# Kernel tuning notes

Hardware: AMD Instinct MI355X
Metric: run time of the kernel (lower is better)

The kernel has to match this reference:

```python
import jax, jax.numpy as jnp
import numpy as np

WH, WW = 7, 7           # window height/width
N = WH * WW             # tokens per window = 49
C = 768                 # num_channels
H = 24                  # num_heads
D = C // H              # head_dim = 32
B = 1024                # total windows (batch * windows-per-image)
NW = 64                 # windows per image (shift_mask leading dim)
EPS = 1e-5


def _relative_position_index():
    # Mirrors the torch buffer construction in __init__.
    coords = np.stack(np.meshgrid(np.arange(WH), np.arange(WW), indexing='ij'))  # [2,WH,WW]
    cf = coords.reshape(2, -1)                          # [2,N]
    rel = cf[:, :, None] - cf[:, None, :]               # [2,N,N]
    rel = rel.transpose(1, 2, 0).copy()                 # [N,N,2]
    rel[:, :, 0] += WH - 1
    rel[:, :, 1] += WW - 1
    rel[:, :, 0] *= 2 * WW - 1
    return jnp.asarray(rel.sum(-1), dtype=jnp.int32)    # [N,N]


def setup_inputs() -> dict:
    key = jax.random.key(0)
    ks = jax.random.split(key, 6)
    x = jax.random.normal(ks[0], (B, N, C), dtype=jnp.float32)
    shift_mask = jax.random.normal(ks[1], (NW, N, N), dtype=jnp.float32)
    w_qkv = jax.random.normal(ks[2], (3 * C, C), dtype=jnp.float32) * 0.02
    b_qkv = jnp.zeros((3 * C,), dtype=jnp.float32)
    w_proj = jax.random.normal(ks[3], (C, C), dtype=jnp.float32) * 0.02
    b_proj = jnp.zeros((C,), dtype=jnp.float32)
    rel_bias_table = jax.random.normal(ks[4], ((2 * WH - 1) * (2 * WW - 1), H), dtype=jnp.float32) * 0.02
    ln_g = jnp.ones((C,), dtype=jnp.float32)
    ln_b = jnp.zeros((C,), dtype=jnp.float32)
    rel_pos_index = _relative_position_index()
    return {
        'x': x, 'shift_mask': shift_mask,
        'w_qkv': w_qkv, 'b_qkv': b_qkv,
        'w_proj': w_proj, 'b_proj': b_proj,
        'rel_bias_table': rel_bias_table,
        'ln_g': ln_g, 'ln_b': ln_b,
        'rel_pos_index': rel_pos_index,
    }


def reference(x, shift_mask, w_qkv, b_qkv, w_proj, b_proj, rel_bias_table, ln_g, ln_b, rel_pos_index):
    B_, N_, C_ = x.shape
    # QKV projection: [B,N,3C] -> [3,B,H,N,D]
    qkv = (x @ w_qkv.T + b_qkv).reshape(B_, N_, 3, H, D).transpose(2, 0, 3, 1, 4)
    q, k, v = qkv[0], qkv[1], qkv[2]
    # Relative position bias gather: [N,N,H] -> [1,H,N,N]
    bias = rel_bias_table[rel_pos_index.reshape(-1)].reshape(N_, N_, H).transpose(2, 0, 1)[None]
    # Shift mask broadcast over batch repeats and heads: [B,1,N,N]
    mask = jnp.tile(shift_mask, (B_ // shift_mask.shape[0], 1, 1))[:, None]
    attn_bias = bias + mask  # [B,H,N,N]
    scale = 1.0 / np.sqrt(D).astype(np.float32)
    scores = jnp.einsum('bhnd,bhmd->bhnm', q, k) * scale + attn_bias
    attn = jax.nn.softmax(scores, axis=-1)
    out = jnp.einsum('bhnm,bhmd->bhnd', attn, v)       # [B,H,N,D]
    out = out.transpose(0, 2, 1, 3).reshape(B_, N_, C_)
    out = out @ w_proj.T + b_proj                      # dropout p=0 -> identity
    y = out + x
    mu = jnp.mean(y, axis=-1, keepdims=True)
    var = jnp.mean(jnp.square(y - mu), axis=-1, keepdims=True)
    return (y - mu) * jax.lax.rsqrt(var + EPS) * ln_g + ln_b
```

## Files before the change

kernel.cpp:

```cpp
#include <hip/hip_runtime.h>
#include <hip/hip_bf16.h>

#define SEQ 49
#define CH 768
#define NH 24
#define HD 32
#define NB 1024
#define NWIN 64
#define MTOT (NB*SEQ)

typedef __hip_bfloat16 bf16;
typedef __attribute__((ext_vector_type(8))) short short8;
typedef __attribute__((ext_vector_type(4))) short short4v;
typedef __attribute__((ext_vector_type(4))) float f32x4;

#define MD  ((size_t)MTOT * HD)
#define NHMD ((size_t)NH * MD)

__device__ __forceinline__ void gload16(const void* g, void* l) {
  __builtin_amdgcn_global_load_lds((__attribute__((address_space(1))) void*)g,
                                   (__attribute__((address_space(3))) void*)l,
                                   16, 0, 0);
}

__device__ __forceinline__ float bf2f(short s) {
  return __uint_as_float(((unsigned int)(unsigned short)s) << 16);
}

__global__ void cvt_bf16(const float* __restrict__ in, bf16* __restrict__ o, int n4) {
  int i = blockIdx.x * blockDim.x + threadIdx.x;
  if (i >= n4) return;
  float4 v = ((const float4*)in)[i];
  union { bf16 b[4]; short4 s; } u;
  u.b[0] = __float2bfloat16(v.x);
  u.b[1] = __float2bfloat16(v.y);
  u.b[2] = __float2bfloat16(v.z);
  u.b[3] = __float2bfloat16(v.w);
  ((short4*)o)[i] = u.s;
}

__global__ void build_comb(const float* __restrict__ table, const int* __restrict__ rpi,
                           const float* __restrict__ smask, bf16* __restrict__ comb) {
  int i = blockIdx.x * blockDim.x + threadIdx.x;
  if (i >= NWIN * NH * 1024) return;
  int idx = i * 4;
  int e0 = idx & 7;
  int l = (idx >> 3) & 63;
  int jj = (idx >> 9) & 7;
  int sh = idx >> 12;
  int h = sh % NH;
  int s = sh / NH;
  union { bf16 b[4]; short4 v; } u;
#pragma unroll
  for (int k = 0; k < 4; k++) {
    int j = jj * 8 + e0 + k;
    int mt = j >> 4, nt = (j >> 2) & 3, r = j & 3;
    int m = 16 * mt + 4 * (l >> 4) + r;
    int n = 16 * nt + (l & 15);
    float v = -1e30f;
    if (m < SEQ && n < SEQ)
      v = (table[rpi[m * SEQ + n] * NH + h] + smask[s * SEQ * SEQ + m * SEQ + n])
          * 1.4426950408889634f;
    u.b[k] = __float2bfloat16(v);
  }
  *(short4*)(comb + idx) = u.v;
}

__global__ __launch_bounds__(512) void qkv_gemm(
    const bf16* __restrict__ A, const bf16* __restrict__ Bw,
    const float* __restrict__ bias, bf16* __restrict__ C)
{
  extern __shared__ __align__(16) bf16 lds[];
  const int tid = threadIdx.x;
  const int w = tid >> 6, l = tid & 63;
  const int lr = l & 15, lg = l >> 4;
  const int wm = w >> 2, wn = w & 3;

  const int flat = blockIdx.x;
  const int xcd = flat & 7, lid = flat >> 3;
  const int wgid = (xcd < 4 ? xcd * 221 : 884 + (xcd - 4) * 220) + lid;
  const int bm = wgid / 9, bn = wgid - 9 * bm;

  const bf16* gA[4];
  const bf16* gB[4];
  int ldst[4];
#pragma unroll
  for (int j = 0; j < 4; j++) {
    int c = j * 512 + tid;
    int row = c >> 3, cpos = c & 7;
    int srcch = cpos ^ (row & 7);
    gA[j] = A + ((size_t)(bm * 256 + row)) * CH + srcch * 8;
    gB[j] = Bw + ((size_t)(bn * 256 + row)) * CH + srcch * 8;
    ldst[j] = c * 8;
  }

  f32x4 acc[8][4];
  f32x4 zero4 = {0.f, 0.f, 0.f, 0.f};
#pragma unroll
  for (int i = 0; i < 8; i++)
#pragma unroll
    for (int j = 0; j < 4; j++) acc[i][j] = zero4;

  int offA[8][2], offB[4][2];
#pragma unroll
  for (int mi = 0; mi < 8; mi++)
#pragma unroll
    for (int ks = 0; ks < 2; ks++) {
      int rowa = wm * 128 + mi * 16 + lr;
      offA[mi][ks] = rowa * 64 + ((lg + 4 * ks) ^ (rowa & 7)) * 8;
    }
#pragma unroll
  for (int nj = 0; nj < 4; nj++)
#pragma unroll
    for (int ks = 0; ks < 2; ks++) {
      int rowb = wn * 64 + nj * 16 + lr;
      offB[nj][ks] = rowb * 64 + ((lg + 4 * ks) ^ (rowb & 7)) * 8;
    }

  gload16(gB[0], lds + 32768 + ldst[0]);
  gload16(gB[1], lds + 32768 + ldst[1]);
  gload16(gB[2], lds + 32768 + ldst[2]);
  gload16(gB[3], lds + 32768 + ldst[3]);
  gload16(gA[0], lds + ldst[0]);
  gload16(gA[2], lds + ldst[2]);
  gload16(gA[1], lds + ldst[1]);
  gload16(gA[3], lds + ldst[3]);

  for (int t = 0; t < 12; ++t) {
    const int cur = t & 1;
    const bf16* cA = lds + cur * 16384;
    const bf16* cB = lds + 32768 + cur * 16384;
    bf16* nA = lds + (cur ^ 1) * 16384;
    bf16* nB = lds + 32768 + (cur ^ 1) * 16384;
    const int kk = (t + 1) * 64;
    const bool pf = (t < 11);
#pragma unroll
    for (int p = 0; p < 4; ++p) {
      const int hp = p >> 1, ks = p & 1;
      if (p == 0) {
        asm volatile("s_waitcnt vmcnt(2)" ::: "memory");
      } else if (p == 2) {
        if (pf) asm volatile("s_waitcnt vmcnt(4)" ::: "memory");
        else    asm volatile("s_waitcnt vmcnt(0)" ::: "memory");
      }
      __builtin_amdgcn_sched_barrier(0);
      __builtin_amdgcn_s_barrier();
      __builtin_amdgcn_sched_barrier(0);
      short8 af[4], bfv[4];
#pragma unroll
      for (int mi = 0; mi < 4; mi++) af[mi] = *(const short8*)(cA + offA[hp * 4 + mi][ks]);
#pragma unroll
      for (int nj = 0; nj < 4; nj++) bfv[nj] = *(const short8*)(cB + offB[nj][ks]);
      if (pf) {
        if (p == 0) { gload16(gB[0] + kk, nB + ldst[0]); gload16(gB[1] + kk, nB + ldst[1]); }
        if (p == 1) { gload16(gB[2] + kk, nB + ldst[2]); gload16(gB[3] + kk, nB + ldst[3]); }
        if (p == 2) { gload16(gA[0] + kk, nA + ldst[0]); gload16(gA[2] + kk, nA + ldst[2]); }
        if (p == 3) { gload16(gA[1] + kk, nA + ldst[1]); gload16(gA[3] + kk, nA + ldst[3]); }
      }
      asm volatile("s_waitcnt lgkmcnt(0)" ::: "memory");
      __builtin_amdgcn_sched_barrier(0);
      __builtin_amdgcn_s_setprio(1);
#pragma unroll
      for (int mi = 0; mi < 4; mi++)
#pragma unroll
        for (int nj = 0; nj < 4; nj++)
          acc[hp * 4 + mi][nj] =
              __builtin_amdgcn_mfma_f32_16x16x32_bf16(af[mi], bfv[nj], acc[hp * 4 + mi][nj], 0, 0, 0);
      __builtin_amdgcn_s_setprio(0);
    }
  }

  const float scale = 0.25503487724583985f;
  const int colbase = bn * 256 + 64 * wn;
  const int rowbase = bm * 256 + 128 * wm;
#pragma unroll
  for (int nj = 0; nj < 4; nj++) {
    const int cb16 = colbase + 16 * nj;
    const int sec = cb16 / 768;
    const int rem = cb16 - sec * 768;
    const int h = rem >> 5;
    const int dbase = rem & 31;
    float bv = bias[cb16 + lr];
    if (sec == 2) {
      const size_t vbase = 2 * NHMD + ((size_t)h * HD + dbase + lr) * MTOT;
#pragma unroll
      for (int mi = 0; mi < 8; mi++) {
        size_t row = rowbase + 16 * mi + 4 * lg;
        union { bf16 b[4]; short4 s; } u;
#pragma unroll
        for (int r = 0; r < 4; r++) u.b[r] = __float2bfloat16(acc[mi][nj][r] + bv);
        *(short4*)(C + vbase + row) = u.s;
      }
    } else {
      const float mul = (sec == 0) ? scale : 1.0f;
      const size_t base = (size_t)sec * NHMD + (size_t)h * MD + dbase + lr;
#pragma unroll
      for (int mi = 0; mi < 8; mi++) {
#pragma unroll
        for (int r = 0; r < 4; r++) {
          size_t row = rowbase + 16 * mi + 4 * lg + r;
          C[base + row * HD] = __float2bfloat16((acc[mi][nj][r] + bv) * mul);
        }
      }
    }
  }
}

__global__ __launch_bounds__(256, 4) void attn_kernel(
    const bf16* __restrict__ qkvT, const bf16* __restrict__ comb,
    bf16* __restrict__ aout)
{
  __shared__ __align__(16) bf16 P[4][64 * 72];
  const int tid = threadIdx.x;
  const int w = tid >> 6, l = tid & 63;
  const int lr = l & 15, lg = l >> 4;
  const int b = blockIdx.x;
  const int h = blockIdx.y * 4 + w;
  const size_t rowb = (size_t)b * SEQ;
  f32x4 zero4 = {0.f, 0.f, 0.f, 0.f};

  const bf16* qb = qkvT + (size_t)h * MD + rowb * HD;
  const bf16* kb = qkvT + NHMD + (size_t)h * MD + rowb * HD;
  const bf16* vT = qkvT + 2 * NHMD + (size_t)h * HD * MTOT;

  short8 kf[4];
#pragma unroll
  for (int nt = 0; nt < 4; nt++)
    kf[nt] = *(const short8*)(kb + (16 * nt + lr) * HD + 8 * lg);

  short8 pb[2][2];
#pragma unroll
  for (int kt = 0; kt < 2; kt++)
#pragma unroll
    for (int dt = 0; dt < 2; dt++)
      pb[kt][dt] = *(const short8*)(vT + ((size_t)(16 * dt + lr)) * MTOT + rowb + 32 * kt + 8 * lg);

  const bf16* cbp = comb + (((size_t)(b & (NWIN - 1)) * NH + h) << 12);
  float inv[4][4];

#pragma unroll
  for (int mt = 0; mt < 4; mt++) {
    short8 qf = *(const short8*)(qb + (16 * mt + lr) * HD + 8 * lg);
    f32x4 s4[4];
#pragma unroll
    for (int nt = 0; nt < 4; nt++)
      s4[nt] = __builtin_amdgcn_mfma_f32_16x16x32_bf16(qf, kf[nt], zero4, 0, 0, 0);
    short8 c0 = *(const short8*)(cbp + ((2 * mt) * 64 + l) * 8);
    short8 c1 = *(const short8*)(cbp + ((2 * mt + 1) * 64 + l) * 8);
#pragma unroll
    for (int e = 0; e < 8; e++) s4[e >> 2][e & 3] += bf2f(c0[e]);
#pragma unroll
    for (int e = 0; e < 8; e++) s4[2 + (e >> 2)][e & 3] += bf2f(c1[e]);
#pragma unroll
    for (int r = 0; r < 4; r++) {
      float t = 0.f;
#pragma unroll
      for (int nt = 0; nt < 4; nt++) {
        float e = exp2f(s4[nt][r]);
        s4[nt][r] = e;
        t += e;
      }
      t += __shfl_xor(t, 1, 64);
      t += __shfl_xor(t, 2, 64);
      t += __shfl_xor(t, 4, 64);
      t += __shfl_xor(t, 8, 64);
      inv[mt][r] = 1.0f / t;
    }
#pragma unroll
    for (int nt = 0; nt < 4; nt++)
#pragma unroll
      for (int r = 0; r < 4; r++)
        P[w][(16 * mt + 4 * lg + r) * 72 + 16 * nt + lr] = __float2bfloat16(s4[nt][r]);
  }

  f32x4 o[4][2];
#pragma unroll
  for (int mt = 0; mt < 4; mt++) { o[mt][0] = zero4; o[mt][1] = zero4; }
#pragma unroll
  for (int kt = 0; kt < 2; kt++) {
    short8 pa[4];
#pragma unroll
    for (int mt = 0; mt < 4; mt++)
      pa[mt] = *(const short8*)(&P[w][(16 * mt + lr) * 72 + 32 * kt + 8 * lg]);
#pragma unroll
    for (int mt = 0; mt < 4; mt++)
#pragma unroll
      for (int dt = 0; dt < 2; dt++)
        o[mt][dt] = __builtin_amdgcn_mfma_f32_16x16x32_bf16(pa[mt], pb[kt][dt], o[mt][dt], 0, 0, 0);
  }

#pragma unroll
  for (int mt = 0; mt < 4; mt++)
#pragma unroll
    for (int dt = 0; dt < 2; dt++)
#pragma unroll
      for (int r = 0; r < 4; r++) {
        int m = 16 * mt + 4 * lg + r;
        if (m < SEQ)
          aout[(rowb + m) * CH + h * HD + 16 * dt + lr] =
              __float2bfloat16(o[mt][dt][r] * inv[mt][r]);
      }
}

__global__ __launch_bounds__(256) void proj_gemm(
    const bf16* __restrict__ A, const bf16* __restrict__ Bw,
    const float* __restrict__ bias, const bf16* __restrict__ xb,
    bf16* __restrict__ Y)
{
  __shared__ __align__(16) bf16 As[2 * 128 * 64];
  __shared__ __align__(16) bf16 Bs[2 * 128 * 64];
  const int tid = threadIdx.x;
  const int w = tid >> 6, l = tid & 63;
  const int lr = l & 15, lg = l >> 4;
  const int wm = w >> 1, wn = w & 1;

  const int flat = blockIdx.x;
  const int wg = (flat & 7) * 294 + (flat >> 3);
  const int bm = wg / 6, bn = wg - 6 * (wg / 6);

  const bf16* gA[4];
  const bf16* gB[4];
  int ldst[4];
#pragma unroll
  for (int j = 0; j < 4; j++) {
    int c = j * 256 + tid;
    int row = c >> 3, cpos = c & 7;
    int srcch = cpos ^ (row & 7);
    gA[j] = A + ((size_t)(bm * 128 + row)) * CH + srcch * 8;
    gB[j] = Bw + ((size_t)(bn * 128 + row)) * CH + srcch * 8;
    ldst[j] = c * 8;
  }

  f32x4 acc[4][4];
  f32x4 zero4 = {0.f, 0.f, 0.f, 0.f};
#pragma unroll
  for (int i = 0; i < 4; i++)
#pragma unroll
    for (int j = 0; j < 4; j++) acc[i][j] = zero4;

  int offA[4][2], offB[4][2];
#pragma unroll
  for (int mi = 0; mi < 4; mi++) {
#pragma unroll
    for (int ks = 0; ks < 2; ks++) {
      int rowa = 64 * wm + 16 * mi + lr;
      offA[mi][ks] = rowa * 64 + ((lg + 4 * ks) ^ (rowa & 7)) * 8;
      int rowb = 64 * wn + 16 * mi + lr;
      offB[mi][ks] = rowb * 64 + ((lg + 4 * ks) ^ (rowb & 7)) * 8;
    }
  }

#pragma unroll
  for (int j = 0; j < 4; j++) gload16(gA[j], As + ldst[j]);
#pragma unroll
  for (int j = 0; j < 4; j++) gload16(gB[j], Bs + ldst[j]);

  for (int t = 0; t < 12; ++t) {
    const int base = (t & 1) * 8192;
    asm volatile("s_waitcnt vmcnt(0)" ::: "memory");
    __builtin_amdgcn_sched_barrier(0);
    __builtin_amdgcn_s_barrier();
    __builtin_amdgcn_sched_barrier(0);
    const bf16* cA = As + base;
    const bf16* cB = Bs + base;
    bf16* nA = As + (base ^ 8192);
    bf16* nB = Bs + (base ^ 8192);
    const int kk = (t + 1) * 64;
    const bool pf = (t < 11);
#pragma unroll
    for (int ks = 0; ks < 2; ks++) {
      short8 af[4], bfv[4];
#pragma unroll
      for (int mi = 0; mi < 4; mi++) {
        af[mi] = *(const short8*)(cA + offA[mi][ks]);
        bfv[mi] = *(const short8*)(cB + offB[mi][ks]);
      }
      if (pf && ks == 0) {
#pragma unroll
        for (int j = 0; j < 4; j++) {
          gload16(gA[j] + kk, nA + ldst[j]);
          gload16(gB[j] + kk, nB + ldst[j]);
        }
      }
      asm volatile("s_waitcnt lgkmcnt(0)" ::: "memory");
      __builtin_amdgcn_sched_barrier(0);
      __builtin_amdgcn_s_setprio(1);
#pragma unroll
      for (int mi = 0; mi < 4; mi++)
#pragma unroll
        for (int nj = 0; nj < 4; nj++)
          acc[mi][nj] = __builtin_amdgcn_mfma_f32_16x16x32_bf16(af[mi], bfv[nj], acc[mi][nj], 0, 0, 0);
      __builtin_amdgcn_s_setprio(0);
    }
  }

  const int colbase = bn * 128 + 64 * wn;
  const int rowbase = bm * 128 + 64 * wm;
#pragma unroll
  for (int nj = 0; nj < 4; nj++) {
    int col = colbase + 16 * nj + lr;
    float bv = bias[col];
#pragma unroll
    for (int mi = 0; mi < 4; mi++) {
#pragma unroll
      for (int r = 0; r < 4; r++) {
        size_t row = rowbase + 16 * mi + 4 * lg + r;
        float v = acc[mi][nj][r] + bv + bf2f(((const short*)xb)[row * CH + col]);
        Y[row * CH + col] = __float2bfloat16(v);
      }
    }
  }
}

__global__ __launch_bounds__(256) void ln_kernel(
    const bf16* __restrict__ Y, const float* __restrict__ g,
    const float* __restrict__ be, float* __restrict__ out)
{
  const int w = threadIdx.x >> 6, l = threadIdx.x & 63;
  const size_t r = (size_t)blockIdx.x * 4 + w;
  const bf16* yr = Y + r * CH;

  short8 a = *(const short8*)(yr + 8 * l);
  short4v b4 = *(const short4v*)(yr + 512 + 4 * l);
  float v[12];
#pragma unroll
  for (int j = 0; j < 8; j++) v[j] = bf2f(a[j]);
#pragma unroll
  for (int j = 0; j < 4; j++) v[8 + j] = bf2f(b4[j]);

  float s1 = 0.f, s2 = 0.f;
#pragma unroll
  for (int j = 0; j < 12; j++) { s1 += v[j]; s2 += v[j] * v[j]; }
#pragma unroll
  for (int m = 1; m <= 32; m <<= 1) {
    s1 += __shfl_xor(s1, m, 64);
    s2 += __shfl_xor(s2, m, 64);
  }
  float mu = s1 * (1.0f / 768.0f);
  float var = s2 * (1.0f / 768.0f) - mu * mu;
  float rs = rsqrtf(var + 1e-5f);

  float4 g0 = *(const float4*)(g + 8 * l);
  float4 g1 = *(const float4*)(g + 8 * l + 4);
  float4 g2 = *(const float4*)(g + 512 + 4 * l);
  float4 b0 = *(const float4*)(be + 8 * l);
  float4 b1 = *(const float4*)(be + 8 * l + 4);
  float4 b2 = *(const float4*)(be + 512 + 4 * l);

  float4 o0, o1, o2;
  o0.x = (v[0] - mu) * rs * g0.x + b0.x;
  o0.y = (v[1] - mu) * rs * g0.y + b0.y;
  o0.z = (v[2] - mu) * rs * g0.z + b0.z;
  o0.w = (v[3] - mu) * rs * g0.w + b0.w;
  o1.x = (v[4] - mu) * rs * g1.x + b1.x;
  o1.y = (v[5] - mu) * rs * g1.y + b1.y;
  o1.z = (v[6] - mu) * rs * g1.z + b1.z;
  o1.w = (v[7] - mu) * rs * g1.w + b1.w;
  o2.x = (v[8] - mu) * rs * g2.x + b2.x;
  o2.y = (v[9] - mu) * rs * g2.y + b2.y;
  o2.z = (v[10] - mu) * rs * g2.z + b2.z;
  o2.w = (v[11] - mu) * rs * g2.w + b2.w;

  float* orow = out + r * CH;
  *(float4*)(orow + 8 * l) = o0;
  *(float4*)(orow + 8 * l + 4) = o1;
  *(float4*)(orow + 512 + 4 * l) = o2;
}

extern "C" void kernel_launch(void* const* d_in, const int* in_sizes, int n_in,
                              void* d_out, int out_size, void* d_ws, size_t ws_size,
                              hipStream_t stream) {
  (void)in_sizes; (void)n_in; (void)out_size; (void)ws_size;
  const float* x     = (const float*)d_in[0];
  const float* smask = (const float*)d_in[1];
  const float* wqkv  = (const float*)d_in[2];
  const float* bqkv  = (const float*)d_in[3];
  const float* wproj = (const float*)d_in[4];
  const float* bproj = (const float*)d_in[5];
  const float* table = (const float*)d_in[6];
  const float* lng   = (const float*)d_in[7];
  const float* lnb   = (const float*)d_in[8];
  const int*   rpi   = (const int*)d_in[9];
  float* out = (float*)d_out;

  char* ws = (char*)d_ws;
  bf16*  xb   = (bf16*)(ws);
  bf16*  wqb  = (bf16*)(ws + 77070336);
  bf16*  wpb  = (bf16*)(ws + 80609280);
  bf16*  comb = (bf16*)(ws + 81788928);
  bf16*  qkvT = (bf16*)(ws + 94371840);
  bf16*  aout = (bf16*)(ws + 325582848);
  bf16*  yb   = (bf16*)(ws + 94371840);

  cvt_bf16<<<37632, 256, 0, stream>>>(x, xb, 9633792);
  cvt_bf16<<<1728, 256, 0, stream>>>(wqkv, wqb, 442368);
  cvt_bf16<<<576, 256, 0, stream>>>(wproj, wpb, 147456);
  build_comb<<<6144, 256, 0, stream>>>(table, rpi, smask, comb);
  qkv_gemm<<<1764, 512, 131072, stream>>>(xb, wqb, bqkv, qkvT);
  attn_kernel<<<dim3(1024, 6), 256, 0, stream>>>(qkvT, comb, aout);
  proj_gemm<<<2352, 256, 0, stream>>>(aout, wpb, bproj, xb, yb);
  ln_kernel<<<12544, 256, 0, stream>>>(yb, lng, lnb, out);
}
```

Measured before the change: 512.7 us.

## Split GEMM k-step into four phases with staggered partial vmcnt waits

The projection GEMM main loop is restructured into four sub-phases per k-tile, each with a barrier. The next tile's global-to-LDS loads are spread across the phases, and the code waits on partial vmcnt counts so MFMA work can begin before the full tile has landed. The attention kernel also hoists all four Q fragment loads ahead of the score loop. The changes trade more barriers and tighter reasoning about load ordering for better overlap of memory and compute, and they risk LDS hazards if the vmcnt counts are wrong.

```diff
diff --git a/kernel.cpp b/kernel.cpp
--- a/kernel.cpp
+++ b/kernel.cpp
@@ -223,7 +223,10 @@
   const bf16* kb = qkvT + NHMD + (size_t)h * MD + rowb * HD;
   const bf16* vT = qkvT + 2 * NHMD + (size_t)h * HD * MTOT;
 
-  short8 kf[4];
+  short8 qf[4], kf[4];
+#pragma unroll
+  for (int mt = 0; mt < 4; mt++)
+    qf[mt] = *(const short8*)(qb + (16 * mt + lr) * HD + 8 * lg);
 #pragma unroll
   for (int nt = 0; nt < 4; nt++)
     kf[nt] = *(const short8*)(kb + (16 * nt + lr) * HD + 8 * lg);
@@ -240,11 +243,10 @@
 
 #pragma unroll
   for (int mt = 0; mt < 4; mt++) {
-    short8 qf = *(const short8*)(qb + (16 * mt + lr) * HD + 8 * lg);
     f32x4 s4[4];
 #pragma unroll
     for (int nt = 0; nt < 4; nt++)
-      s4[nt] = __builtin_amdgcn_mfma_f32_16x16x32_bf16(qf, kf[nt], zero4, 0, 0, 0);
+      s4[nt] = __builtin_amdgcn_mfma_f32_16x16x32_bf16(qf[mt], kf[nt], zero4, 0, 0, 0);
     short8 c0 = *(const short8*)(cbp + ((2 * mt) * 64 + l) * 8);
     short8 c1 = *(const short8*)(cbp + ((2 * mt + 1) * 64 + l) * 8);
 #pragma unroll
@@ -350,17 +352,17 @@
     }
   }
 
-#pragma unroll
-  for (int j = 0; j < 4; j++) gload16(gA[j], As + ldst[j]);
-#pragma unroll
-  for (int j = 0; j < 4; j++) gload16(gB[j], Bs + ldst[j]);
+  gload16(gB[0], Bs + ldst[0]);
+  gload16(gB[1], Bs + ldst[1]);
+  gload16(gB[2], Bs + ldst[2]);
+  gload16(gB[3], Bs + ldst[3]);
+  gload16(gA[0], As + ldst[0]);
+  gload16(gA[2], As + ldst[2]);
+  gload16(gA[1], As + ldst[1]);
+  gload16(gA[3], As + ldst[3]);
 
   for (int t = 0; t < 12; ++t) {
     const int base = (t & 1) * 8192;
-    asm volatile("s_waitcnt vmcnt(0)" ::: "memory");
-    __builtin_amdgcn_sched_barrier(0);
-    __builtin_amdgcn_s_barrier();
-    __builtin_amdgcn_sched_barrier(0);
     const bf16* cA = As + base;
     const bf16* cB = Bs + base;
     bf16* nA = As + (base ^ 8192);
@@ -368,28 +370,37 @@
     const int kk = (t + 1) * 64;
     const bool pf = (t < 11);
 #pragma unroll
-    for (int ks = 0; ks < 2; ks++) {
-      short8 af[4], bfv[4];
-#pragma unroll
-      for (int mi = 0; mi < 4; mi++) {
-        af[mi] = *(const short8*)(cA + offA[mi][ks]);
-        bfv[mi] = *(const short8*)(cB + offB[mi][ks]);
-      }
-      if (pf && ks == 0) {
-#pragma unroll
-        for (int j = 0; j < 4; j++) {
-          gload16(gA[j] + kk, nA + ldst[j]);
-          gload16(gB[j] + kk, nB + ldst[j]);
-        }
+    for (int p = 0; p < 4; ++p) {
+      const int hp = p >> 1, ks = p & 1;
+      if (p == 0) {
+        asm volatile("s_waitcnt vmcnt(2)" ::: "memory");
+      } else if (p == 2) {
+        if (pf) asm volatile("s_waitcnt vmcnt(4)" ::: "memory");
+        else    asm volatile("s_waitcnt vmcnt(0)" ::: "memory");
+      }
+      __builtin_amdgcn_sched_barrier(0);
+      __builtin_amdgcn_s_barrier();
+      __builtin_amdgcn_sched_barrier(0);
+      short8 af[2], bfv[4];
+#pragma unroll
+      for (int i = 0; i < 2; i++) af[i] = *(const short8*)(cA + offA[hp * 2 + i][ks]);
+#pragma unroll
+      for (int nj = 0; nj < 4; nj++) bfv[nj] = *(const short8*)(cB + offB[nj][ks]);
+      if (pf) {
+        if (p == 0) { gload16(gB[0] + kk, nB + ldst[0]); gload16(gB[1] + kk, nB + ldst[1]); }
+        if (p == 1) { gload16(gB[2] + kk, nB + ldst[2]); gload16(gB[3] + kk, nB + ldst[3]); }
+        if (p == 2) { gload16(gA[0] + kk, nA + ldst[0]); gload16(gA[2] + kk, nA + ldst[2]); }
+        if (p == 3) { gload16(gA[1] + kk, nA + ldst[1]); gload16(gA[3] + kk, nA + ldst[3]); }
       }
       asm volatile("s_waitcnt lgkmcnt(0)" ::: "memory");
       __builtin_amdgcn_sched_barrier(0);
       __builtin_amdgcn_s_setprio(1);
 #pragma unroll
-      for (int mi = 0; mi < 4; mi++)
+      for (int i = 0; i < 2; i++)
 #pragma unroll
         for (int nj = 0; nj < 4; nj++)
-          acc[mi][nj] = __builtin_amdgcn_mfma_f32_16x16x32_bf16(af[mi], bfv[nj], acc[mi][nj], 0, 0, 0);
+          acc[hp * 2 + i][nj] =
+              __builtin_amdgcn_mfma_f32_16x16x32_bf16(af[i], bfv[nj], acc[hp * 2 + i][nj], 0, 0, 0);
       __builtin_amdgcn_s_setprio(0);
     }
   }
```

Measured after the change: 533.8 us. +4.1%, slower.
